# Optimization experiments

Hardware: AMD Instinct MI355X
Metric: run time of the kernel (lower is better)

The kernel has to match this reference:

```python
import jax, jax.numpy as jnp
import numpy as np

B = 32768
HID = 64
IU = np.triu_indices(9)  # 45 upper-triangular (incl. diagonal) entries of a 9x9 matrix
DIAG = np.arange(9)


def setup_inputs() -> dict:
    key = jax.random.key(0)
    ks = jax.random.split(key, 12)
    return {
        "x": jax.random.normal(ks[0], (B, 1, 9, 7), jnp.float32),
        "adj": jax.random.randint(ks[1], (B, 45), 0, 2, jnp.int32),
        "context": jax.random.normal(ks[2], (B, 1, 9, 5), jnp.float32),
        # DenseGCNConv(7, 7): linear weight + bias
        "gcn_W": jax.random.normal(ks[3], (7, 7), jnp.float32) * 0.3,
        "gcn_b": jax.random.normal(ks[4], (7,), jnp.float32) * 0.05,
        # context_net Linear(45, 63)
        "ctx_W": jax.random.normal(ks[5], (45, 63), jnp.float32) * 0.15,
        "ctx_b": jax.random.normal(ks[6], (63,), jnp.float32) * 0.05,
        # three 1x1 convs: 2->64, 64->64, 64->2 (weights stored [out, in])
        "W1": jax.random.normal(ks[7], (HID, 2), jnp.float32) * 0.5,
        "b1": jnp.zeros((HID,), jnp.float32),
        "W2": jax.random.normal(ks[8], (HID, HID), jnp.float32) * 0.12,
        "b2": jnp.zeros((HID,), jnp.float32),
        "W3": jax.random.normal(ks[9], (2, HID), jnp.float32) * 0.12,
        "b3": jnp.zeros((2,), jnp.float32),
    }


def reference(x, adj, context, gcn_W, gcn_b, ctx_W, ctx_b, W1, b1, W2, b2, W3, b3):
    Bn = x.shape[0]
    # scatter 45 edge values into the upper triangle of a [B,9,9] adjacency, binarize
    A = jnp.zeros((Bn, 9, 9), jnp.float32).at[:, IU[0], IU[1]].set(adj.astype(jnp.float32))
    A = (A > 0.0).astype(jnp.float32)
    # DenseGCNConv: add self-loops (diag := 1), symmetric degree normalization
    A = A.at[:, DIAG, DIAG].set(1.0)
    d = jnp.maximum(A.sum(-1), 1.0) ** -0.5  # [B,9]
    An = d[:, :, None] * A * d[:, None, :]
    z = x[:, 0]  # [B,9,7]
    z = jnp.einsum('bnm,bmf->bnf', An, z @ gcn_W) + gcn_b  # [B,9,7]
    # context MLP: flatten -> Linear(45,63) -> ReLU -> reshape (9,7)
    c = jax.nn.relu(context.reshape(Bn, 1, 45) @ ctx_W + ctx_b).reshape(Bn, 1, 9, 7)
    h = jnp.concatenate([z[:, None], c], axis=1)  # [B,2,9,7]
    # 1x1 conv stack == per-pixel channel GEMMs
    h = jax.nn.relu(jnp.einsum('bchw,oc->bohw', h, W1) + b1[:, None, None])
    h = jax.nn.relu(jnp.einsum('bchw,oc->bohw', h, W2) + b2[:, None, None])
    return jnp.einsum('bchw,oc->bohw', h, W3) + b3[:, None, None]  # [B,2,9,7]
```

## Files before the change

### kernel.cpp

```cpp
#include <hip/hip_runtime.h>
#include <cstdint>

#define BLOCK_SIZE 256
#define NPOS 63

typedef __attribute__((ext_vector_type(8))) _Float16 f16x8;
typedef __attribute__((ext_vector_type(4))) float f32x4;
typedef __attribute__((ext_vector_type(4))) unsigned int uint4v;

__device__ __forceinline__ unsigned rne_f16(float a) {
    _Float16 h = (_Float16)a;
    return (unsigned)__builtin_bit_cast(unsigned short, h);
}
__device__ __forceinline__ unsigned pack_f16(float a, float b) {
    auto t = __builtin_amdgcn_cvt_pkrtz(a, b);
    return __builtin_bit_cast(unsigned, t);
}

__global__ __launch_bounds__(BLOCK_SIZE) void carnet_fused(
    const float* __restrict__ x,
    const int*   __restrict__ adj,
    const float* __restrict__ ctx,
    const float* __restrict__ gcn_W,
    const float* __restrict__ gcn_b,
    const float* __restrict__ ctx_W,
    const float* __restrict__ ctx_b,
    const float* __restrict__ W1,
    const float* __restrict__ b1,
    const float* __restrict__ W2,
    const float* __restrict__ b2,
    const float* __restrict__ W3,
    const float* __restrict__ b3,
    float* __restrict__ out)
{
    __shared__ short sh2b[64 * 64];

    const int t    = threadIdx.x;
    const int lane = t & 63;

    {
        const int r  = t >> 2;
        const int cq = t & 3;
        const float* wsrc = W2 + r * 64 + cq * 16;
        const float4 w0 = ((const float4*)wsrc)[0];
        const float4 w1 = ((const float4*)wsrc)[1];
        const float4 w2v = ((const float4*)wsrc)[2];
        const float4 w3v = ((const float4*)wsrc)[3];
        uint4v hA = { rne_f16(w0.x)  | (rne_f16(w0.y)  << 16),
                      rne_f16(w0.z)  | (rne_f16(w0.w)  << 16),
                      rne_f16(w1.x)  | (rne_f16(w1.y)  << 16),
                      rne_f16(w1.z)  | (rne_f16(w1.w)  << 16) };
        uint4v hB = { rne_f16(w2v.x) | (rne_f16(w2v.y) << 16),
                      rne_f16(w2v.z) | (rne_f16(w2v.w) << 16),
                      rne_f16(w3v.x) | (rne_f16(w3v.y) << 16),
                      rne_f16(w3v.z) | (rne_f16(w3v.w) << 16) };
        const int sA = ((2 * cq)     ^ (r & 7)) * 8;
        const int sB = ((2 * cq + 1) ^ (r & 7)) * 8;
        *(uint4v*)&sh2b[r * 64 + sA] = hA;
        *(uint4v*)&sh2b[r * 64 + sB] = hB;
    }

    const int b = __builtin_amdgcn_readfirstlane(blockIdx.x * 4 + (t >> 6));
    const int p = lane < 63 ? lane : 62;
    const int n = p / 7;
    const int f = p - n * 7;

    const int* ab = adj + b * 45;
    int aval = 0;
    if (lane < 45) aval = ab[lane];
    const uint64_t am = __ballot(aval != 0);

    float d[9];
#pragma unroll
    for (int i = 0; i < 9; ++i) {
        const int s = 9 * i - (i * (i - 1)) / 2;
        const int w = 8 - i;
        const uint64_t bits = (am >> (s + 1)) & ((1ull << w) - 1ull);
        d[i] = __frsqrt_rn((float)(1 + __popcll(bits)));
    }

    const float* xb = x + b * 63;
    float yv = 0.f;
#pragma unroll
    for (int k = 0; k < 7; ++k)
        yv = fmaf(xb[n * 7 + k], gcn_W[k * 7 + f], yv);

    float zt = 0.f;
    const int snn = 9 * n - (n * (n - 1)) / 2 - n;
#pragma unroll
    for (int m = 0; m < 9; ++m) {
        const float ym = __shfl(yv, m * 7 + f);
        int sh = snn + m;
        sh = sh < 0 ? 0 : sh;
        const bool conn = (m == n) || ((m > n) && ((am >> sh) & 1ull));
        zt = fmaf(conn ? d[m] : 0.f, ym, zt);
    }
    const float zv = fmaf(d[n], zt, gcn_b[f]);

    const float* cb = ctx + b * 45;
    float ca0 = ctx_b[p], ca1 = 0.f, ca2 = 0.f, ca3 = 0.f;
#pragma unroll
    for (int q = 0; q < 44; q += 4) {
        ca0 = fmaf(cb[q],     ctx_W[q * 63 + p],       ca0);
        ca1 = fmaf(cb[q + 1], ctx_W[(q + 1) * 63 + p], ca1);
        ca2 = fmaf(cb[q + 2], ctx_W[(q + 2) * 63 + p], ca2);
        ca3 = fmaf(cb[q + 3], ctx_W[(q + 3) * 63 + p], ca3);
    }
    ca0 = fmaf(cb[44], ctx_W[44 * 63 + p], ca0);
    const float cvv = fmaxf((ca0 + ca1) + (ca2 + ca3), 0.f);

    const int cl   = lane & 15;
    const int quad = lane >> 4;
    const int s0 = (quad ^ (cl & 7)) * 16;

    float2 wp0[8], wp1[8];
    float  bb0[8], bb1[8];
#pragma unroll
    for (int j = 0; j < 8; ++j) {
        const int o = quad * 8 + j;
        wp0[j] = *(const float2*)(W1 + 2 * o);
        bb0[j] = b1[o];
        wp1[j] = *(const float2*)(W1 + 2 * (o + 32));
        bb1[j] = b1[o + 32];
    }

    const float4 b2q0 = *(const float4*)(b2 + quad * 4);
    const float4 b2q1 = *(const float4*)(b2 + 16 + quad * 4);
    const float4 b2q2 = *(const float4*)(b2 + 32 + quad * 4);
    const float4 b2q3 = *(const float4*)(b2 + 48 + quad * 4);
    const float4 wa0 = *(const float4*)(W3 + quad * 4);
    const float4 wa1 = *(const float4*)(W3 + 16 + quad * 4);
    const float4 wa2 = *(const float4*)(W3 + 32 + quad * 4);
    const float4 wa3 = *(const float4*)(W3 + 48 + quad * 4);
    const float4 wb0 = *(const float4*)(W3 + 64 + quad * 4);
    const float4 wb1 = *(const float4*)(W3 + 80 + quad * 4);
    const float4 wb2 = *(const float4*)(W3 + 96 + quad * 4);
    const float4 wb3 = *(const float4*)(W3 + 112 + quad * 4);
    const float b30 = b3[0], b31 = b3[1];
    float* __restrict__ ob = out + b * 126;

    const char* sh2bB = (const char*)sh2b;

    __syncthreads();

#pragma unroll 2
    for (int i = 0; i < 4; ++i) {
        const float zm = __shfl(zv,  i * 16 + cl);
        const float cm = __shfl(cvv, i * 16 + cl);

        uint4v ph0, ph1;
#pragma unroll
        for (int jj = 0; jj < 4; ++jj) {
            float ha = fmaxf(fmaf(wp0[2*jj].x,   zm, fmaf(wp0[2*jj].y,   cm, bb0[2*jj])),   0.f);
            float hb = fmaxf(fmaf(wp0[2*jj+1].x, zm, fmaf(wp0[2*jj+1].y, cm, bb0[2*jj+1])), 0.f);
            ph0[jj] = pack_f16(ha, hb);

            ha = fmaxf(fmaf(wp1[2*jj].x,   zm, fmaf(wp1[2*jj].y,   cm, bb1[2*jj])),   0.f);
            hb = fmaxf(fmaf(wp1[2*jj+1].x, zm, fmaf(wp1[2*jj+1].y, cm, bb1[2*jj+1])), 0.f);
            ph1[jj] = pack_f16(ha, hb);
        }
        const f16x8 ah0 = __builtin_bit_cast(f16x8, ph0);
        const f16x8 ah1 = __builtin_bit_cast(f16x8, ph1);

        f32x4 acc0 = {b2q0.x, b2q0.y, b2q0.z, b2q0.w};
        f32x4 acc1 = {b2q1.x, b2q1.y, b2q1.z, b2q1.w};
        f32x4 acc2 = {b2q2.x, b2q2.y, b2q2.z, b2q2.w};
        f32x4 acc3 = {b2q3.x, b2q3.y, b2q3.z, b2q3.w};

#define STEP(nt) {                                                                    \
        int bo = cl * 128 + s0;                                                       \
        asm volatile("" : "+v"(bo));                                                  \
        const int bo2 = (cl * 128) | (s0 ^ 64);                                       \
        const f16x8 wf0 = *(const f16x8*)(sh2bB + bo  + ((nt) * 2048));               \
        const f16x8 wf1 = *(const f16x8*)(sh2bB + bo2 + ((nt) * 2048));               \
        acc##nt = __builtin_amdgcn_mfma_f32_16x16x32_f16(wf0, ah0, acc##nt, 0, 0, 0); \
        acc##nt = __builtin_amdgcn_mfma_f32_16x16x32_f16(wf1, ah1, acc##nt, 0, 0, 0); }
        STEP(0) STEP(1) STEP(2) STEP(3)
#undef STEP

        float q0, q1;
        {
            float h;
            h = fmaxf(acc0[0], 0.f); q0 = h * wa0.x;            q1 = h * wb0.x;
            h = fmaxf(acc0[1], 0.f); q0 = fmaf(h, wa0.y, q0);   q1 = fmaf(h, wb0.y, q1);
            h = fmaxf(acc0[2], 0.f); q0 = fmaf(h, wa0.z, q0);   q1 = fmaf(h, wb0.z, q1);
            h = fmaxf(acc0[3], 0.f); q0 = fmaf(h, wa0.w, q0);   q1 = fmaf(h, wb0.w, q1);
            h = fmaxf(acc1[0], 0.f); q0 = fmaf(h, wa1.x, q0);   q1 = fmaf(h, wb1.x, q1);
            h = fmaxf(acc1[1], 0.f); q0 = fmaf(h, wa1.y, q0);   q1 = fmaf(h, wb1.y, q1);
            h = fmaxf(acc1[2], 0.f); q0 = fmaf(h, wa1.z, q0);   q1 = fmaf(h, wb1.z, q1);
            h = fmaxf(acc1[3], 0.f); q0 = fmaf(h, wa1.w, q0);   q1 = fmaf(h, wb1.w, q1);
            h = fmaxf(acc2[0], 0.f); q0 = fmaf(h, wa2.x, q0);   q1 = fmaf(h, wb2.x, q1);
            h = fmaxf(acc2[1], 0.f); q0 = fmaf(h, wa2.y, q0);   q1 = fmaf(h, wb2.y, q1);
            h = fmaxf(acc2[2], 0.f); q0 = fmaf(h, wa2.z, q0);   q1 = fmaf(h, wb2.z, q1);
            h = fmaxf(acc2[3], 0.f); q0 = fmaf(h, wa2.w, q0);   q1 = fmaf(h, wb2.w, q1);
            h = fmaxf(acc3[0], 0.f); q0 = fmaf(h, wa3.x, q0);   q1 = fmaf(h, wb3.x, q1);
            h = fmaxf(acc3[1], 0.f); q0 = fmaf(h, wa3.y, q0);   q1 = fmaf(h, wb3.y, q1);
            h = fmaxf(acc3[2], 0.f); q0 = fmaf(h, wa3.z, q0);   q1 = fmaf(h, wb3.z, q1);
            h = fmaxf(acc3[3], 0.f); q0 = fmaf(h, wa3.w, q0);   q1 = fmaf(h, wb3.w, q1);
        }
        q0 += __shfl_xor(q0, 16); q0 += __shfl_xor(q0, 32);
        q1 += __shfl_xor(q1, 16); q1 += __shfl_xor(q1, 32);

        const int pp = i * 16 + cl;
        if (quad == 0 && pp < NPOS) {
            ob[pp]        = q0 + b30;
            ob[NPOS + pp] = q1 + b31;
        }
    }
}

extern "C" void kernel_launch(void* const* d_in, const int* in_sizes, int n_in,
                              void* d_out, int out_size, void* d_ws, size_t ws_size,
                              hipStream_t stream) {
    const float* x     = (const float*)d_in[0];
    const int*   adj   = (const int*)  d_in[1];
    const float* ctx   = (const float*)d_in[2];
    const float* gcn_W = (const float*)d_in[3];
    const float* gcn_b = (const float*)d_in[4];
    const float* ctx_W = (const float*)d_in[5];
    const float* ctx_b = (const float*)d_in[6];
    const float* W1    = (const float*)d_in[7];
    const float* b1    = (const float*)d_in[8];
    const float* W2    = (const float*)d_in[9];
    const float* b2    = (const float*)d_in[10];
    const float* W3    = (const float*)d_in[11];
    const float* b3    = (const float*)d_in[12];
    float* out = (float*)d_out;

    const int nbatch = in_sizes[1] / 45;
    const int grid = (nbatch + 3) / 4;
    carnet_fused<<<grid, BLOCK_SIZE, 0, stream>>>(
        x, adj, ctx, gcn_W, gcn_b, ctx_W, ctx_b,
        W1, b1, W2, b2, W3, b3, out);
}
```

Before: 164.9 us.

## Process two batch items per wavefront to amortize W2 staging and interleave MFMAs

Each wavefront now handles two batch elements instead of one, so each block covers 8 items and the grid is halved. This spreads the per-block W2 fp16 conversion into shared memory, the weight/bias register loads, and the shared-memory W2 fragment reads over twice the work. It also interleaves two independent MFMA chains to hide their latency. The costs are higher register pressure, the loss of the unroll-2 on the position loop, and fewer blocks in flight.

```diff
diff --git a/kernel.cpp b/kernel.cpp
--- a/kernel.cpp
+++ b/kernel.cpp
@@ -3,6 +3,7 @@
 
 #define BLOCK_SIZE 256
 #define NPOS 63
+#define BPB  8
 
 typedef __attribute__((ext_vector_type(8))) _Float16 f16x8;
 typedef __attribute__((ext_vector_type(4))) float f32x4;
@@ -31,7 +32,8 @@
     const float* __restrict__ b2,
     const float* __restrict__ W3,
     const float* __restrict__ b3,
-    float* __restrict__ out)
+    float* __restrict__ out,
+    const int nbatch)
 {
     __shared__ short sh2b[64 * 64];
 
@@ -60,54 +62,80 @@
         *(uint4v*)&sh2b[r * 64 + sB] = hB;
     }
 
-    const int b = __builtin_amdgcn_readfirstlane(blockIdx.x * 4 + (t >> 6));
+    const int bA = __builtin_amdgcn_readfirstlane(blockIdx.x * BPB + (t >> 6));
+    const int bBr = bA + 4;
+    const bool hasB = (bBr < nbatch);
+    const int bB = __builtin_amdgcn_readfirstlane(hasB ? bBr : bA);
+
     const int p = lane < 63 ? lane : 62;
     const int n = p / 7;
     const int f = p - n * 7;
 
-    const int* ab = adj + b * 45;
-    int aval = 0;
-    if (lane < 45) aval = ab[lane];
-    const uint64_t am = __ballot(aval != 0);
-
-    float d[9];
+    const int* abA = adj + bA * 45;
+    const int* abB = adj + bB * 45;
+    int avA = 0, avB = 0;
+    if (lane < 45) { avA = abA[lane]; avB = abB[lane]; }
+    const uint64_t amA = __ballot(avA != 0);
+    const uint64_t amB = __ballot(avB != 0);
+
+    float dA[9], dB[9];
 #pragma unroll
     for (int i = 0; i < 9; ++i) {
         const int s = 9 * i - (i * (i - 1)) / 2;
-        const int w = 8 - i;
-        const uint64_t bits = (am >> (s + 1)) & ((1ull << w) - 1ull);
-        d[i] = __frsqrt_rn((float)(1 + __popcll(bits)));
-    }
-
-    const float* xb = x + b * 63;
-    float yv = 0.f;
-#pragma unroll
-    for (int k = 0; k < 7; ++k)
-        yv = fmaf(xb[n * 7 + k], gcn_W[k * 7 + f], yv);
-
-    float zt = 0.f;
+        const uint64_t mk = (1ull << (8 - i)) - 1ull;
+        dA[i] = __frsqrt_rn((float)(1 + __popcll((amA >> (s + 1)) & mk)));
+        dB[i] = __frsqrt_rn((float)(1 + __popcll((amB >> (s + 1)) & mk)));
+    }
+
+    const float* xbA = x + bA * 63;
+    const float* xbB = x + bB * 63;
+    float yA = 0.f, yB = 0.f;
+#pragma unroll
+    for (int k = 0; k < 7; ++k) {
+        const float g = gcn_W[k * 7 + f];
+        yA = fmaf(xbA[n * 7 + k], g, yA);
+        yB = fmaf(xbB[n * 7 + k], g, yB);
+    }
+
+    float zA0 = 0.f, zA1 = 0.f, zA2 = 0.f, zB0 = 0.f, zB1 = 0.f, zB2 = 0.f;
     const int snn = 9 * n - (n * (n - 1)) / 2 - n;
 #pragma unroll
     for (int m = 0; m < 9; ++m) {
-        const float ym = __shfl(yv, m * 7 + f);
+        const float ymA = __shfl(yA, m * 7 + f);
+        const float ymB = __shfl(yB, m * 7 + f);
         int sh = snn + m;
         sh = sh < 0 ? 0 : sh;
-        const bool conn = (m == n) || ((m > n) && ((am >> sh) & 1ull));
-        zt = fmaf(conn ? d[m] : 0.f, ym, zt);
-    }
-    const float zv = fmaf(d[n], zt, gcn_b[f]);
-
-    const float* cb = ctx + b * 45;
-    float ca0 = ctx_b[p], ca1 = 0.f, ca2 = 0.f, ca3 = 0.f;
+        const bool up = (m > n);
+        const float tA = ((m == n) || (up && ((amA >> sh) & 1ull))) ? dA[m] : 0.f;
+        const float tB = ((m == n) || (up && ((amB >> sh) & 1ull))) ? dB[m] : 0.f;
+        if (m < 3)      { zA0 = fmaf(tA, ymA, zA0); zB0 = fmaf(tB, ymB, zB0); }
+        else if (m < 6) { zA1 = fmaf(tA, ymA, zA1); zB1 = fmaf(tB, ymB, zB1); }
+        else            { zA2 = fmaf(tA, ymA, zA2); zB2 = fmaf(tB, ymB, zB2); }
+    }
+    const float gbf = gcn_b[f];
+    const float zvA = fmaf(dA[n], (zA0 + zA1) + zA2, gbf);
+    const float zvB = fmaf(dB[n], (zB0 + zB1) + zB2, gbf);
+
+    const float* cbA = ctx + bA * 45;
+    const float* cbB = ctx + bB * 45;
+    const float cb0 = ctx_b[p];
+    float aA0 = cb0, aA1 = 0.f, aA2 = 0.f, aA3 = 0.f;
+    float aB0 = cb0, aB1 = 0.f, aB2 = 0.f, aB3 = 0.f;
 #pragma unroll
     for (int q = 0; q < 44; q += 4) {
-        ca0 = fmaf(cb[q],     ctx_W[q * 63 + p],       ca0);
-        ca1 = fmaf(cb[q + 1], ctx_W[(q + 1) * 63 + p], ca1);
-        ca2 = fmaf(cb[q + 2], ctx_W[(q + 2) * 63 + p], ca2);
-        ca3 = fmaf(cb[q + 3], ctx_W[(q + 3) * 63 + p], ca3);
-    }
-    ca0 = fmaf(cb[44], ctx_W[44 * 63 + p], ca0);
-    const float cvv = fmaxf((ca0 + ca1) + (ca2 + ca3), 0.f);
+        const float w0 = ctx_W[q * 63 + p];
+        const float w1 = ctx_W[(q + 1) * 63 + p];
+        const float w2 = ctx_W[(q + 2) * 63 + p];
+        const float w3 = ctx_W[(q + 3) * 63 + p];
+        aA0 = fmaf(cbA[q],     w0, aA0);  aB0 = fmaf(cbB[q],     w0, aB0);
+        aA1 = fmaf(cbA[q + 1], w1, aA1);  aB1 = fmaf(cbB[q + 1], w1, aB1);
+        aA2 = fmaf(cbA[q + 2], w2, aA2);  aB2 = fmaf(cbB[q + 2], w2, aB2);
+        aA3 = fmaf(cbA[q + 3], w3, aA3);  aB3 = fmaf(cbB[q + 3], w3, aB3);
+    }
+    const float w44 = ctx_W[44 * 63 + p];
+    aA0 = fmaf(cbA[44], w44, aA0);  aB0 = fmaf(cbB[44], w44, aB0);
+    const float cvA = fmaxf((aA0 + aA1) + (aA2 + aA3), 0.f);
+    const float cvB = fmaxf((aB0 + aB1) + (aB2 + aB3), 0.f);
 
     const int cl   = lane & 15;
     const int quad = lane >> 4;
@@ -137,75 +165,97 @@
     const float4 wb2 = *(const float4*)(W3 + 96 + quad * 4);
     const float4 wb3 = *(const float4*)(W3 + 112 + quad * 4);
     const float b30 = b3[0], b31 = b3[1];
-    float* __restrict__ ob = out + b * 126;
-
-    const char* sh2bB = (const char*)sh2b;
+    float* __restrict__ obA = out + bA * 126;
+    float* __restrict__ obB = out + bB * 126;
+
+    const char* sh2bB_ = (const char*)sh2b;
 
     __syncthreads();
 
-#pragma unroll 2
+    auto epilogue = [&](const f32x4& a0, const f32x4& a1,
+                        const f32x4& a2, const f32x4& a3,
+                        float* obp, int pp, bool valid) {
+        float q0, q1, h;
+        h = fmaxf(a0[0], 0.f); q0 = h * wa0.x;            q1 = h * wb0.x;
+        h = fmaxf(a0[1], 0.f); q0 = fmaf(h, wa0.y, q0);   q1 = fmaf(h, wb0.y, q1);
+        h = fmaxf(a0[2], 0.f); q0 = fmaf(h, wa0.z, q0);   q1 = fmaf(h, wb0.z, q1);
+        h = fmaxf(a0[3], 0.f); q0 = fmaf(h, wa0.w, q0);   q1 = fmaf(h, wb0.w, q1);
+        h = fmaxf(a1[0], 0.f); q0 = fmaf(h, wa1.x, q0);   q1 = fmaf(h, wb1.x, q1);
+        h = fmaxf(a1[1], 0.f); q0 = fmaf(h, wa1.y, q0);   q1 = fmaf(h, wb1.y, q1);
+        h = fmaxf(a1[2], 0.f); q0 = fmaf(h, wa1.z, q0);   q1 = fmaf(h, wb1.z, q1);
+        h = fmaxf(a1[3], 0.f); q0 = fmaf(h, wa1.w, q0);   q1 = fmaf(h, wb1.w, q1);
+        h = fmaxf(a2[0], 0.f); q0 = fmaf(h, wa2.x, q0);   q1 = fmaf(h, wb2.x, q1);
+        h = fmaxf(a2[1], 0.f); q0 = fmaf(h, wa2.y, q0);   q1 = fmaf(h, wb2.y, q1);
+        h = fmaxf(a2[2], 0.f); q0 = fmaf(h, wa2.z, q0);   q1 = fmaf(h, wb2.z, q1);
+        h = fmaxf(a2[3], 0.f); q0 = fmaf(h, wa2.w, q0);   q1 = fmaf(h, wb2.w, q1);
+        h = fmaxf(a3[0], 0.f); q0 = fmaf(h, wa3.x, q0);   q1 = fmaf(h, wb3.x, q1);
+        h = fmaxf(a3[1], 0.f); q0 = fmaf(h, wa3.y, q0);   q1 = fmaf(h, wb3.y, q1);
+        h = fmaxf(a3[2], 0.f); q0 = fmaf(h, wa3.z, q0);   q1 = fmaf(h, wb3.z, q1);
+        h = fmaxf(a3[3], 0.f); q0 = fmaf(h, wa3.w, q0);   q1 = fmaf(h, wb3.w, q1);
+        q0 += __shfl_xor(q0, 16); q0 += __shfl_xor(q0, 32);
+        q1 += __shfl_xor(q1, 16); q1 += __shfl_xor(q1, 32);
+        if (quad == 0 && pp < NPOS && valid) {
+            obp[pp]        = q0 + b30;
+            obp[NPOS + pp] = q1 + b31;
+        }
+    };
+
+#pragma unroll 1
     for (int i = 0; i < 4; ++i) {
-        const float zm = __shfl(zv,  i * 16 + cl);
-        const float cm = __shfl(cvv, i * 16 + cl);
-
-        uint4v ph0, ph1;
+        const float zmA = __shfl(zvA, i * 16 + cl);
+        const float cmA = __shfl(cvA, i * 16 + cl);
+        const float zmB = __shfl(zvB, i * 16 + cl);
+        const float cmB = __shfl(cvB, i * 16 + cl);
+
+        uint4v pA0, pA1, pB0, pB1;
 #pragma unroll
         for (int jj = 0; jj < 4; ++jj) {
-            float ha = fmaxf(fmaf(wp0[2*jj].x,   zm, fmaf(wp0[2*jj].y,   cm, bb0[2*jj])),   0.f);
-            float hb = fmaxf(fmaf(wp0[2*jj+1].x, zm, fmaf(wp0[2*jj+1].y, cm, bb0[2*jj+1])), 0.f);
-            ph0[jj] = pack_f16(ha, hb);
-
-            ha = fmaxf(fmaf(wp1[2*jj].x,   zm, fmaf(wp1[2*jj].y,   cm, bb1[2*jj])),   0.f);
-            hb = fmaxf(fmaf(wp1[2*jj+1].x, zm, fmaf(wp1[2*jj+1].y, cm, bb1[2*jj+1])), 0.f);
-            ph1[jj] = pack_f16(ha, hb);
+            const float2 u0 = wp0[2*jj],   u1 = wp0[2*jj+1];
+            const float2 v0 = wp1[2*jj],   v1 = wp1[2*jj+1];
+            const float  c0 = bb0[2*jj],   c1 = bb0[2*jj+1];
+            const float  e0 = bb1[2*jj],   e1 = bb1[2*jj+1];
+
+            float ha = fmaxf(fmaf(u0.x, zmA, fmaf(u0.y, cmA, c0)), 0.f);
+            float hb = fmaxf(fmaf(u1.x, zmA, fmaf(u1.y, cmA, c1)), 0.f);
+            pA0[jj] = pack_f16(ha, hb);
+            ha = fmaxf(fmaf(v0.x, zmA, fmaf(v0.y, cmA, e0)), 0.f);
+            hb = fmaxf(fmaf(v1.x, zmA, fmaf(v1.y, cmA, e1)), 0.f);
+            pA1[jj] = pack_f16(ha, hb);
+
+            ha = fmaxf(fmaf(u0.x, zmB, fmaf(u0.y, cmB, c0)), 0.f);
+            hb = fmaxf(fmaf(u1.x, zmB, fmaf(u1.y, cmB, c1)), 0.f);
+            pB0[jj] = pack_f16(ha, hb);
+            ha = fmaxf(fmaf(v0.x, zmB, fmaf(v0.y, cmB, e0)), 0.f);
+            hb = fmaxf(fmaf(v1.x, zmB, fmaf(v1.y, cmB, e1)), 0.f);
+            pB1[jj] = pack_f16(ha, hb);
         }
-        const f16x8 ah0 = __builtin_bit_cast(f16x8, ph0);
-        const f16x8 ah1 = __builtin_bit_cast(f16x8, ph1);
-
-        f32x4 acc0 = {b2q0.x, b2q0.y, b2q0.z, b2q0.w};
-        f32x4 acc1 = {b2q1.x, b2q1.y, b2q1.z, b2q1.w};
-        f32x4 acc2 = {b2q2.x, b2q2.y, b2q2.z, b2q2.w};
-        f32x4 acc3 = {b2q3.x, b2q3.y, b2q3.z, b2q3.w};
-
-#define STEP(nt) {                                                                    \
-        int bo = cl * 128 + s0;                                                       \
-        asm volatile("" : "+v"(bo));                                                  \
-        const int bo2 = (cl * 128) | (s0 ^ 64);                                       \
-        const f16x8 wf0 = *(const f16x8*)(sh2bB + bo  + ((nt) * 2048));               \
-        const f16x8 wf1 = *(const f16x8*)(sh2bB + bo2 + ((nt) * 2048));               \
-        acc##nt = __builtin_amdgcn_mfma_f32_16x16x32_f16(wf0, ah0, acc##nt, 0, 0, 0); \
-        acc##nt = __builtin_amdgcn_mfma_f32_16x16x32_f16(wf1, ah1, acc##nt, 0, 0, 0); }
+        const f16x8 ahA0 = __builtin_bit_cast(f16x8, pA0);
+        const f16x8 ahA1 = __builtin_bit_cast(f16x8, pA1);
+        const f16x8 ahB0 = __builtin_bit_cast(f16x8, pB0);
+        const f16x8 ahB1 = __builtin_bit_cast(f16x8, pB1);
+
+        f32x4 accA0 = {b2q0.x, b2q0.y, b2q0.z, b2q0.w};
+        f32x4 accA1 = {b2q1.x, b2q1.y, b2q1.z, b2q1.w};
+        f32x4 accA2 = {b2q2.x, b2q2.y, b2q2.z, b2q2.w};
+        f32x4 accA3 = {b2q3.x, b2q3.y, b2q3.z, b2q3.w};
+        f32x4 accB0 = accA0, accB1 = accA1, accB2 = accA2, accB3 = accA3;
+
+#define STEP(nt) {                                                                      \
+        int bo = cl * 128 + s0;                                                         \
+        asm volatile("" : "+v"(bo));                                                    \
+        const int bo2 = (cl * 128) | (s0 ^ 64);                                         \
+        const f16x8 wf0 = *(const f16x8*)(sh2bB_ + bo  + ((nt) * 2048));                \
+        const f16x8 wf1 = *(const f16x8*)(sh2bB_ + bo2 + ((nt) * 2048));                \
+        accA##nt = __builtin_amdgcn_mfma_f32_16x16x32_f16(wf0, ahA0, accA##nt, 0, 0, 0); \
+        accB##nt = __builtin_amdgcn_mfma_f32_16x16x32_f16(wf0, ahB0, accB##nt, 0, 0, 0); \
+        accA##nt = __builtin_amdgcn_mfma_f32_16x16x32_f16(wf1, ahA1, accA##nt, 0, 0, 0); \
+        accB##nt = __builtin_amdgcn_mfma_f32_16x16x32_f16(wf1, ahB1, accB##nt, 0, 0, 0); }
         STEP(0) STEP(1) STEP(2) STEP(3)
 #undef STEP
 
-        float q0, q1;
-        {
-            float h;
-            h = fmaxf(acc0[0], 0.f); q0 = h * wa0.x;            q1 = h * wb0.x;
-            h = fmaxf(acc0[1], 0.f); q0 = fmaf(h, wa0.y, q0);   q1 = fmaf(h, wb0.y, q1);
-            h = fmaxf(acc0[2], 0.f); q0 = fmaf(h, wa0.z, q0);   q1 = fmaf(h, wb0.z, q1);
-            h = fmaxf(acc0[3], 0.f); q0 = fmaf(h, wa0.w, q0);   q1 = fmaf(h, wb0.w, q1);
-            h = fmaxf(acc1[0], 0.f); q0 = fmaf(h, wa1.x, q0);   q1 = fmaf(h, wb1.x, q1);
-            h = fmaxf(acc1[1], 0.f); q0 = fmaf(h, wa1.y, q0);   q1 = fmaf(h, wb1.y, q1);
-            h = fmaxf(acc1[2], 0.f); q0 = fmaf(h, wa1.z, q0);   q1 = fmaf(h, wb1.z, q1);
-            h = fmaxf(acc1[3], 0.f); q0 = fmaf(h, wa1.w, q0);   q1 = fmaf(h, wb1.w, q1);
-            h = fmaxf(acc2[0], 0.f); q0 = fmaf(h, wa2.x, q0);   q1 = fmaf(h, wb2.x, q1);
-            h = fmaxf(acc2[1], 0.f); q0 = fmaf(h, wa2.y, q0);   q1 = fmaf(h, wb2.y, q1);
-            h = fmaxf(acc2[2], 0.f); q0 = fmaf(h, wa2.z, q0);   q1 = fmaf(h, wb2.z, q1);
-            h = fmaxf(acc2[3], 0.f); q0 = fmaf(h, wa2.w, q0);   q1 = fmaf(h, wb2.w, q1);
-            h = fmaxf(acc3[0], 0.f); q0 = fmaf(h, wa3.x, q0);   q1 = fmaf(h, wb3.x, q1);
-            h = fmaxf(acc3[1], 0.f); q0 = fmaf(h, wa3.y, q0);   q1 = fmaf(h, wb3.y, q1);
-            h = fmaxf(acc3[2], 0.f); q0 = fmaf(h, wa3.z, q0);   q1 = fmaf(h, wb3.z, q1);
-            h = fmaxf(acc3[3], 0.f); q0 = fmaf(h, wa3.w, q0);   q1 = fmaf(h, wb3.w, q1);
-        }
-        q0 += __shfl_xor(q0, 16); q0 += __shfl_xor(q0, 32);
-        q1 += __shfl_xor(q1, 16); q1 += __shfl_xor(q1, 32);
-
         const int pp = i * 16 + cl;
-        if (quad == 0 && pp < NPOS) {
-            ob[pp]        = q0 + b30;
-            ob[NPOS + pp] = q1 + b31;
-        }
+        epilogue(accA0, accA1, accA2, accA3, obA, pp, true);
+        epilogue(accB0, accB1, accB2, accB3, obB, pp, hasB);
     }
 }
 
@@ -228,8 +278,8 @@
     float* out = (float*)d_out;
 
     const int nbatch = in_sizes[1] / 45;
-    const int grid = (nbatch + 3) / 4;
+    const int grid = (nbatch + BPB - 1) / BPB;
     carnet_fused<<<grid, BLOCK_SIZE, 0, stream>>>(
         x, adj, ctx, gcn_W, gcn_b, ctx_W, ctx_b,
-        W1, b1, W2, b2, W3, b3, out);
-}
+        W1, b1, W2, b2, W3, b3, out, nbatch);
+}
```

Result: faster. 146.4 us (-11.2%).
